# Kernel optimization log

Measured on AMD Instinct MI355X. Metric: run time of the kernel, lower is better.

The kernel has to match this reference:

```python
import jax, jax.numpy as jnp
import numpy as np

B = 32768
E = 10  # number of motion experts


def _p(k, shape, scale=0.05):
    return jax.random.normal(k, shape, dtype=jnp.float32) * scale


def setup_inputs() -> dict:
    key = jax.random.key(0)
    ks = jax.random.split(key, 24)
    inp = {"input_": jax.random.normal(ks[0], (B, 556), dtype=jnp.float32)}
    # encoder 0: pose 400 -> 512 -> 512
    inp["e0_W0"] = _p(ks[1], (400, 512)); inp["e0_b0"] = jnp.zeros((512,), jnp.float32)
    inp["e0_W1"] = _p(ks[2], (512, 512)); inp["e0_b1"] = jnp.zeros((512,), jnp.float32)
    # encoder 1: goal 78 -> 128 -> 128
    inp["e1_W0"] = _p(ks[3], (78, 128)); inp["e1_b0"] = jnp.zeros((128,), jnp.float32)
    inp["e1_W1"] = _p(ks[4], (128, 128)); inp["e1_b1"] = jnp.zeros((128,), jnp.float32)
    # gating NN (1 expert => plain MLP): 78 -> 512 -> 512 -> 10, softmax
    inp["g_W0"] = _p(ks[5], (78, 512)); inp["g_b0"] = jnp.zeros((512,), jnp.float32)
    inp["g_W1"] = _p(ks[6], (512, 512)); inp["g_b1"] = jnp.zeros((512,), jnp.float32)
    inp["g_W2"] = _p(ks[7], (512, 10)); inp["g_b2"] = jnp.zeros((10,), jnp.float32)
    # motion prediction ComponentNN: 10 experts, 640 -> 512 -> 512 -> 578
    inp["m_W0"] = _p(ks[8], (E, 640, 512)); inp["m_b0"] = jnp.zeros((E, 512), jnp.float32)
    inp["m_W1"] = _p(ks[9], (E, 512, 512)); inp["m_b1"] = jnp.zeros((E, 512), jnp.float32)
    inp["m_W2"] = _p(ks[10], (E, 512, 578)); inp["m_b2"] = jnp.zeros((E, 578), jnp.float32)
    return inp


def _expert_layer(x, w, W, b):
    # sum_e w[b,e] * (x[b] @ W[e] + b[e]); blend outputs (equiv. to blending weights)
    return jnp.einsum('be,bi,eio->bo', w, x, W) + w @ b


def reference(input_, e0_W0, e0_b0, e0_W1, e0_b1, e1_W0, e1_b0, e1_W1, e1_b1,
              g_W0, g_b0, g_W1, g_b1, g_W2, g_b2,
              m_W0, m_b0, m_W1, m_b1, m_W2, m_b2):
    elu = jax.nn.elu
    pose = input_[:, 0:400]
    goal = input_[:, 400:478]
    gate_in = input_[:, 478:556]
    # encoders (dropout inactive at inference)
    h0 = elu(elu(pose @ e0_W0 + e0_b0) @ e0_W1 + e0_b1)   # [B,512]
    h1 = elu(elu(goal @ e1_W0 + e1_b0) @ e1_W1 + e1_b1)   # [B,128]
    # gating: softmax over 10 experts
    g = elu(gate_in @ g_W0 + g_b0)
    g = elu(g @ g_W1 + g_b1)
    w = jax.nn.softmax(g @ g_W2 + g_b2, axis=-1)          # [B,10]
    feat = jnp.concatenate([h0, h1], axis=-1)             # [B,640]
    x = elu(_expert_layer(feat, w, m_W0, m_b0))
    x = elu(_expert_layer(x, w, m_W1, m_b1))
    pred = _expert_layer(x, w, m_W2, m_b2)                # [B,578], linear final
    return pred
```

## Files before the change

### kernel.cpp

```cpp
#include <hip/hip_runtime.h>
#include <math.h>

typedef _Float16 h8 __attribute__((ext_vector_type(8)));
typedef float f4 __attribute__((ext_vector_type(4)));

#define BATCH 32768

__device__ __forceinline__ void gload16(const void* g, void* l) {
  __builtin_amdgcn_global_load_lds(
      (const __attribute__((address_space(1))) unsigned int*)g,
      (__attribute__((address_space(3))) unsigned int*)l, 16, 0, 0);
}

__global__ __launch_bounds__(256) void prep_input2_k(const float* __restrict__ in,
    _Float16* __restrict__ pose, _Float16* __restrict__ goal, _Float16* __restrict__ gate)
{
  const long long total = (long long)BATCH * 88;
  for (long long i = (long long)blockIdx.x * 256 + threadIdx.x; i < total;
       i += (long long)gridDim.x * 256) {
    const int b = (int)(i / 88);
    const int g = (int)(i % 88);
    const float* r = in + (size_t)b * 556;
    h8 v;
    if (g < 56) {
      const int c0 = g * 8;
      #pragma unroll
      for (int j = 0; j < 8; ++j) {
        const int c = c0 + j;
        v[j] = (_Float16)((c < 400) ? r[c] : (c == 400 ? 1.0f : 0.0f));
      }
      *reinterpret_cast<h8*>(pose + (size_t)b * 448 + c0) = v;
    } else if (g < 72) {
      const int c0 = (g - 56) * 8;
      #pragma unroll
      for (int j = 0; j < 8; ++j) {
        const int c = c0 + j;
        v[j] = (_Float16)((c < 78) ? r[400 + c] : (c == 78 ? 1.0f : 0.0f));
      }
      *reinterpret_cast<h8*>(goal + (size_t)b * 128 + c0) = v;
    } else {
      const int c0 = (g - 72) * 8;
      #pragma unroll
      for (int j = 0; j < 8; ++j) {
        const int c = c0 + j;
        v[j] = (_Float16)((c < 78) ? r[478 + c] : (c == 78 ? 1.0f : 0.0f));
      }
      *reinterpret_cast<h8*>(gate + (size_t)b * 128 + c0) = v;
    }
  }
}

__global__ __launch_bounds__(256) void prep_wt_k(const float* __restrict__ W,
    const float* __restrict__ bias, _Float16* __restrict__ out,
    int K, int N, int Nld, int Kout, int biasCols, int biasLd)
{
  __shared__ float tile[64 * 65];
  const int t = threadIdx.x;
  const int c0 = blockIdx.x * 64;
  const int n0 = blockIdx.y * 64;
  {
    const int nn = t & 63;
    #pragma unroll
    for (int i = 0; i < 16; ++i) {
      int cc = (t >> 6) + i * 4;
      int c = c0 + cc, n = n0 + nn;
      float v = 0.0f;
      if (n < N) {
        if (c < K) v = W[(size_t)c * Nld + n];
        else if (c - K < biasCols) v = bias[(size_t)(c - K) * biasLd + n];
      }
      tile[cc * 65 + nn] = v;
    }
  }
  __syncthreads();
  {
    const int cc = t & 63;
    #pragma unroll
    for (int i = 0; i < 16; ++i) {
      int nn = (t >> 6) + i * 4;
      out[(size_t)(n0 + nn) * Kout + c0 + cc] = (_Float16)tile[cc * 65 + nn];
    }
  }
}

template<bool EPI_BIAS, bool DO_ELU, bool OUT_F32>
__global__ __launch_bounds__(256, 2) void gemm_k(
    const _Float16* __restrict__ A, const _Float16* __restrict__ Bw,
    void* __restrict__ OutP, const float* __restrict__ bias,
    int ldA, int ldB, int ldO, int nChunks, int nLimit)
{
  __shared__ __align__(16) _Float16 As[2][128 * 64];
  __shared__ __align__(16) _Float16 Bs[2][128 * 64];

  const int t = threadIdx.x;
  const int m0 = blockIdx.x * 128;
  const int n0 = blockIdx.y * 128;
  const int wid = t >> 6;
  const int lane = t & 63;
  const int wm = (wid >> 1) * 64;
  const int wn = (wid & 1) * 64;
  const int lr = lane & 15;
  const int lg = lane >> 4;

  const int gr = lane >> 3;
  const int gcol = ((lane & 7) ^ gr) * 8;
  const _Float16* Abase = A + (size_t)(m0 + wid * 32 + gr) * ldA + gcol;
  const _Float16* Bbase = Bw + (size_t)(n0 + wid * 32 + gr) * ldB + gcol;

  f4 acc[4][4];
  #pragma unroll
  for (int i = 0; i < 4; ++i)
    #pragma unroll
    for (int j = 0; j < 4; ++j) { f4 z = {0.f, 0.f, 0.f, 0.f}; acc[i][j] = z; }

  auto issue = [&](int c, int buf) {
    #pragma unroll
    for (int i = 0; i < 4; ++i) {
      gload16(Abase + (size_t)(i * 8) * ldA + c * 64, &As[buf][(wid * 32 + i * 8) * 64]);
      gload16(Bbase + (size_t)(i * 8) * ldB + c * 64, &Bs[buf][(wid * 32 + i * 8) * 64]);
    }
  };

  auto mfma_step = [&](const _Float16* as, const _Float16* bs) {
    #pragma unroll
    for (int kk = 0; kk < 2; ++kk) {
      h8 af[4], bf[4];
      const int kslot = kk * 4 + lg;
      #pragma unroll
      for (int i = 0; i < 4; ++i) {
        const int row = wm + i * 16 + lr;
        af[i] = *reinterpret_cast<const h8*>(&as[row * 64 + ((kslot ^ (row & 7)) << 3)]);
      }
      #pragma unroll
      for (int j = 0; j < 4; ++j) {
        const int row = wn + j * 16 + lr;
        bf[j] = *reinterpret_cast<const h8*>(&bs[row * 64 + ((kslot ^ (row & 7)) << 3)]);
      }
      #pragma unroll
      for (int i = 0; i < 4; ++i)
        #pragma unroll
        for (int j = 0; j < 4; ++j)
          acc[i][j] = __builtin_amdgcn_mfma_f32_16x16x32_f16(af[i], bf[j], acc[i][j], 0, 0, 0);
    }
  };

  issue(0, 0);
  int cur = 0;
  for (int c = 0; c < nChunks; ++c) {
    __syncthreads();
    if (c + 1 < nChunks) issue(c + 1, cur ^ 1);
    mfma_step(As[cur], Bs[cur]);
    cur ^= 1;
  }

  #pragma unroll
  for (int j = 0; j < 4; ++j) {
    const int col = n0 + wn + j * 16 + lr;
    if (col >= nLimit) continue;
    float bvv = 0.0f;
    if (EPI_BIAS) bvv = bias[col];
    #pragma unroll
    for (int i = 0; i < 4; ++i) {
      const int rowb = m0 + wm + i * 16 + lg * 4;
      #pragma unroll
      for (int r = 0; r < 4; ++r) {
        float x = acc[i][j][r] + bvv;
        if (DO_ELU) x = (x > 0.0f) ? x : expm1f(x);
        if (OUT_F32)
          reinterpret_cast<float*>(OutP)[(size_t)(rowb + r) * ldO + col] = x;
        else
          reinterpret_cast<_Float16*>(OutP)[(size_t)(rowb + r) * ldO + col] = (_Float16)x;
      }
    }
  }
}

template<int KCe, bool DO_ELU, bool OUT_F32>
__global__ __launch_bounds__(256, 4) void expertH_k(
    const _Float16* __restrict__ A, const _Float16* __restrict__ Bw,
    void* __restrict__ OutP, const _Float16* __restrict__ wpad,
    int ldA, int ldB, int ldO, int nLimit)
{
  constexpr int E = 10;
  __shared__ __align__(16) _Float16 lds[16384 + 1280];
  _Float16* Bs = lds;
  _Float16* wT = lds + 16384;

  const int tid = threadIdx.x;
  const int w = tid >> 6;
  const int l = tid & 63;
  const int m0 = blockIdx.x * 128;
  const int n0 = blockIdx.y * 128;
  const int lr = l & 15;
  const int lg = l >> 4;

  const int strow = tid >> 3;
  const int scol = ((tid & 7) ^ (strow & 7)) * 8;

  auto stB = [&](int buf, size_t colEl) {
    _Float16* d = Bs + buf * 8192 + w * 512;
    const _Float16* s = Bw + (size_t)(n0 + strow) * ldB + colEl + scol;
    #pragma unroll
    for (int p = 0; p < 4; ++p)
      gload16(s + (size_t)(p * 32) * ldB, d + p * 2048);
  };

  auto frag = [&](const _Float16* base, int row, int kslot) -> h8 {
    return *reinterpret_cast<const h8*>(base + row * 64 + ((kslot ^ (row & 7)) << 3));
  };

  h8 araw[2][2];
  auto loadA = [&](const _Float16* base, size_t ld, size_t col0) {
    #pragma unroll
    for (int kk = 0; kk < 2; ++kk)
      #pragma unroll
      for (int mi = 0; mi < 2; ++mi)
        araw[kk][mi] = *reinterpret_cast<const h8*>(
            base + (size_t)(m0 + w * 32 + mi * 16 + lr) * ld + col0 + (size_t)(kk * 4 + lg) * 8);
  };

  f4 acc[2][8];
  #pragma unroll
  for (int mi = 0; mi < 2; ++mi)
    #pragma unroll
    for (int ni = 0; ni < 8; ++ni) { f4 z = {0.f, 0.f, 0.f, 0.f}; acc[mi][ni] = z; }

  #pragma unroll
  for (int idx = tid; idx < 1280; idx += 256) {
    const int m = idx & 127, e = idx >> 7;
    wT[e * 128 + m] = wpad[(size_t)(m0 + m) * 64 + e];
  }
  loadA(A, (size_t)ldA, 0);
  stB(0, 0);
  asm volatile("s_waitcnt vmcnt(0) lgkmcnt(0)" ::: "memory");
  __builtin_amdgcn_s_barrier();
  __builtin_amdgcn_sched_barrier(0);

  int s = 0;
  #pragma unroll 1
  for (int kc = 0; kc < KCe; ++kc) {
    #pragma unroll 1
    for (int e = 0; e < E; ++e, ++s) {
      const _Float16* Bh = Bs + (s & 1) * 8192;

      if (e + 1 < E)         stB((s + 1) & 1, (size_t)((e + 1) * KCe + kc) * 64);
      else if (kc + 1 < KCe) stB((s + 1) & 1, (size_t)(kc + 1) * 64);
      else                   stB((s + 1) & 1, (size_t)(E * KCe) * 64);
      __builtin_amdgcn_sched_barrier(0);

      _Float16 se[2];
      #pragma unroll
      for (int j = 0; j < 2; ++j) se[j] = wT[e * 128 + w * 32 + j * 16 + lr];

      #pragma unroll
      for (int kk = 0; kk < 2; ++kk) {
        h8 aa[2];
        #pragma unroll
        for (int mi = 0; mi < 2; ++mi) {
          h8 v = araw[kk][mi];
          const _Float16 sv = se[mi];
          #pragma unroll
          for (int q = 0; q < 8; ++q) v[q] = v[q] * sv;
          aa[mi] = v;
        }
        #pragma unroll
        for (int c0 = 0; c0 < 8; c0 += 4) {
          h8 bf[4];
          #pragma unroll
          for (int ni = 0; ni < 4; ++ni)
            bf[ni] = frag(Bh, (c0 + ni) * 16 + lr, kk * 4 + lg);
          __builtin_amdgcn_s_setprio(1);
          #pragma unroll
          for (int mi = 0; mi < 2; ++mi)
            #pragma unroll
            for (int ni = 0; ni < 4; ++ni)
              acc[mi][c0 + ni] =
                  __builtin_amdgcn_mfma_f32_16x16x32_f16(aa[mi], bf[ni], acc[mi][c0 + ni], 0, 0, 0);
          __builtin_amdgcn_s_setprio(0);
        }
      }

      __builtin_amdgcn_sched_barrier(0);
      asm volatile("s_waitcnt vmcnt(0)" ::: "memory");
      __builtin_amdgcn_s_barrier();
      __builtin_amdgcn_sched_barrier(0);
    }
    if (kc + 1 < KCe) loadA(A, (size_t)ldA, (size_t)(kc + 1) * 64);
    else              loadA(wpad, 64, 0);
  }

  {
    const _Float16* Bh = Bs + (s & 1) * 8192;
    #pragma unroll
    for (int kk = 0; kk < 2; ++kk) {
      #pragma unroll
      for (int c0 = 0; c0 < 8; c0 += 4) {
        h8 bf[4];
        #pragma unroll
        for (int ni = 0; ni < 4; ++ni)
          bf[ni] = frag(Bh, (c0 + ni) * 16 + lr, kk * 4 + lg);
        #pragma unroll
        for (int mi = 0; mi < 2; ++mi)
          #pragma unroll
          for (int ni = 0; ni < 4; ++ni)
            acc[mi][c0 + ni] =
                __builtin_amdgcn_mfma_f32_16x16x32_f16(araw[kk][mi], bf[ni], acc[mi][c0 + ni], 0, 0, 0);
      }
    }
  }

  #pragma unroll
  for (int ni = 0; ni < 8; ++ni) {
    const int col = n0 + ni * 16 + lr;
    if (col >= nLimit) continue;
    #pragma unroll
    for (int mi = 0; mi < 2; ++mi) {
      const int rowb = m0 + w * 32 + mi * 16 + lg * 4;
      #pragma unroll
      for (int r = 0; r < 4; ++r) {
        float x = acc[mi][ni][r];
        if (DO_ELU) x = (x > 0.0f) ? x : expm1f(x);
        if (OUT_F32)
          reinterpret_cast<float*>(OutP)[(size_t)(rowb + r) * ldO + col] = x;
        else
          reinterpret_cast<_Float16*>(OutP)[(size_t)(rowb + r) * ldO + col] = (_Float16)x;
      }
    }
  }
}

template<int KCe, int NI, bool DO_ELU, bool OUT_F32>
__global__ __launch_bounds__(256, 2) void expertV_k(
    const _Float16* __restrict__ A, const _Float16* __restrict__ Bw,
    void* __restrict__ OutP, const _Float16* __restrict__ wpad,
    int ldA, int ldB, int ldO, int nLimit)
{
  constexpr int E = 10;
  constexpr int S = KCe * E + 1;
  constexpr int SG = NI / 2;
  constexpr int SLOT = NI * 1024;
  __shared__ __align__(16) _Float16 lds[3 * SLOT + 2560];
  _Float16* wT = lds + 3 * SLOT;

  const int tid = threadIdx.x;
  const int w = tid >> 6;
  const int l = tid & 63;
  const int m0 = blockIdx.x * 256;
  const int n0 = blockIdx.y * (NI * 16);
  const int lr = l & 15;
  const int lg = l >> 4;

  const int strow = tid >> 3;
  const int scol = ((tid & 7) ^ (strow & 7)) * 8;

  auto stB = [&](int slot, size_t colEl) {
    _Float16* d = lds + slot * SLOT + w * 512;
    const _Float16* sp = Bw + (size_t)(n0 + strow) * ldB + colEl + scol;
    #pragma unroll
    for (int p = 0; p < SG; ++p)
      gload16(sp + (size_t)(p * 32) * ldB, d + p * 2048);
  };

  auto frag = [&](const _Float16* base, int row, int kslot) -> h8 {
    return *reinterpret_cast<const h8*>(base + row * 64 + ((kslot ^ (row & 7)) << 3));
  };

  h8 araw[2][4];
  auto loadA = [&](const _Float16* base, size_t ld, size_t col0) {
    #pragma unroll
    for (int kk = 0; kk < 2; ++kk)
      #pragma unroll
      for (int mi = 0; mi < 4; ++mi)
        araw[kk][mi] = *reinterpret_cast<const h8*>(
            base + (size_t)(m0 + w * 64 + mi * 16 + lr) * ld + col0 + (size_t)(kk * 4 + lg) * 8);
  };

  f4 acc[4][NI];
  #pragma unroll
  for (int mi = 0; mi < 4; ++mi)
    #pragma unroll
    for (int ni = 0; ni < NI; ++ni) { f4 z = {0.f, 0.f, 0.f, 0.f}; acc[mi][ni] = z; }

  #pragma unroll
  for (int idx = tid; idx < 2560; idx += 256) {
    const int m = idx & 255, e = idx >> 8;
    wT[e * 256 + m] = wpad[(size_t)(m0 + m) * 64 + e];
  }
  loadA(A, (size_t)ldA, 0);
  stB(0, 0);
  stB(1, (size_t)KCe * 64);
  if constexpr (SG == 4) asm volatile("s_waitcnt vmcnt(4)" ::: "memory");
  else                   asm volatile("s_waitcnt vmcnt(5)" ::: "memory");
  asm volatile("s_waitcnt lgkmcnt(0)" ::: "memory");
  __builtin_amdgcn_s_barrier();
  __builtin_amdgcn_sched_barrier(0);

  int e_s = 0, kc_s = 0;
  int e_t = 2, kc_t = 0;
  #pragma unroll 1
  for (int s = 0; s < S; ++s) {
    const _Float16* Bh = lds + (s % 3) * SLOT;

    if (s + 2 < S) {
      const size_t col = (kc_t < KCe) ? (size_t)(e_t * KCe + kc_t) * 64
                                      : (size_t)(E * KCe) * 64;
      stB((s + 2) % 3, col);
    }
    __builtin_amdgcn_sched_barrier(0);

    const bool isBias = (kc_s == KCe);
    _Float16 se[4];
    if (!isBias) {
      #pragma unroll
      for (int j = 0; j < 4; ++j) se[j] = wT[e_s * 256 + w * 64 + j * 16 + lr];
    }

    #pragma unroll
    for (int kk = 0; kk < 2; ++kk) {
      h8 aa[4];
      #pragma unroll
      for (int mi = 0; mi < 4; ++mi) {
        h8 v = araw[kk][mi];
        if (!isBias) {
          const _Float16 sv = se[mi];
          #pragma unroll
          for (int q = 0; q < 8; ++q) v[q] = v[q] * sv;
        }
        aa[mi] = v;
      }
      #pragma unroll
      for (int c0 = 0; c0 < NI; c0 += 4) {
        h8 bf[4];
        #pragma unroll
        for (int ni = 0; ni < 4; ++ni)
          if (c0 + ni < NI) bf[ni] = frag(Bh, (c0 + ni) * 16 + lr, kk * 4 + lg);
        __builtin_amdgcn_s_setprio(1);
        #pragma unroll
        for (int mi = 0; mi < 4; ++mi)
          #pragma unroll
          for (int ni = 0; ni < 4; ++ni)
            if (c0 + ni < NI)
              acc[mi][c0 + ni] =
                  __builtin_amdgcn_mfma_f32_16x16x32_f16(aa[mi], bf[ni], acc[mi][c0 + ni], 0, 0, 0);
        __builtin_amdgcn_s_setprio(0);
      }
    }
    __builtin_amdgcn_sched_barrier(0);

    if (s + 1 < S) {
      if (s + 2 < S) {
        if constexpr (SG == 4) asm volatile("s_waitcnt vmcnt(4)" ::: "memory");
        else                   asm volatile("s_waitcnt vmcnt(5)" ::: "memory");
      } else {
        asm volatile("s_waitcnt vmcnt(0)" ::: "memory");
      }
      __builtin_amdgcn_s_barrier();
      __builtin_amdgcn_sched_barrier(0);
      if (e_s == E - 1) {
        if (kc_s + 1 < KCe) loadA(A, (size_t)ldA, (size_t)(kc_s + 1) * 64);
        else                loadA(wpad, 64, 0);
        e_s = 0; ++kc_s;
      } else ++e_s;
      if (kc_t < KCe) { if (e_t == E - 1) { e_t = 0; ++kc_t; } else ++e_t; }
    }
  }

  #pragma unroll
  for (int ni = 0; ni < NI; ++ni) {
    const int col = n0 + ni * 16 + lr;
    if (col >= nLimit) continue;
    #pragma unroll
    for (int mi = 0; mi < 4; ++mi) {
      const int rowb = m0 + w * 64 + mi * 16 + lg * 4;
      #pragma unroll
      for (int r = 0; r < 4; ++r) {
        float x = acc[mi][ni][r];
        if (DO_ELU) x = (x > 0.0f) ? x : expm1f(x);
        if (OUT_F32)
          reinterpret_cast<float*>(OutP)[(size_t)(rowb + r) * ldO + col] = x;
        else
          reinterpret_cast<_Float16*>(OutP)[(size_t)(rowb + r) * ldO + col] = (_Float16)x;
      }
    }
  }
}

__global__ __launch_bounds__(256) void gate_softmax_k(const _Float16* __restrict__ gb,
    const float* __restrict__ W2, const float* __restrict__ b2, _Float16* __restrict__ wpad)
{
  __shared__ float W2s[5120];
  for (int i = threadIdx.x; i < 5120; i += 256) W2s[i] = W2[i];
  __syncthreads();
  const int t = threadIdx.x;
  const int sub = t & 3;
  const int b = blockIdx.x * 64 + (t >> 2);
  const _Float16* row = gb + (size_t)b * 512 + sub * 128;
  float acc[10];
  #pragma unroll
  for (int o = 0; o < 10; ++o) acc[o] = 0.0f;
  #pragma unroll 4
  for (int k0 = 0; k0 < 128; k0 += 8) {
    h8 x = *reinterpret_cast<const h8*>(row + k0);
    #pragma unroll
    for (int jj = 0; jj < 8; ++jj) {
      float xv = (float)x[jj];
      const int k = sub * 128 + k0 + jj;
      #pragma unroll
      for (int o = 0; o < 10; ++o) acc[o] += xv * W2s[k * 10 + o];
    }
  }
  #pragma unroll
  for (int o = 0; o < 10; ++o) {
    acc[o] += __shfl_xor(acc[o], 1);
    acc[o] += __shfl_xor(acc[o], 2);
    acc[o] += b2[o];
  }
  float mx = acc[0];
  #pragma unroll
  for (int o = 1; o < 10; ++o) mx = fmaxf(mx, acc[o]);
  float s = 0.0f;
  #pragma unroll
  for (int o = 0; o < 10; ++o) { acc[o] = expf(acc[o] - mx); s += acc[o]; }
  const float inv = 1.0f / s;
  h8 o0 = {0,0,0,0,0,0,0,0}, o1 = {0,0,0,0,0,0,0,0};
  if (sub == 0) {
    #pragma unroll
    for (int o = 0; o < 8; ++o) o0[o] = (_Float16)(acc[o] * inv);
    o1[0] = (_Float16)(acc[8] * inv);
    o1[1] = (_Float16)(acc[9] * inv);
  }
  _Float16* wr = wpad + (size_t)b * 64 + sub * 16;
  *reinterpret_cast<h8*>(wr) = o0;
  *reinterpret_cast<h8*>(wr + 8) = o1;
}

extern "C" void kernel_launch(void* const* d_in, const int* in_sizes, int n_in,
                              void* d_out, int out_size, void* d_ws, size_t ws_size,
                              hipStream_t stream)
{
  const float* input_ = (const float*)d_in[0];
  const float* e0_W0 = (const float*)d_in[1];
  const float* e0_b0 = (const float*)d_in[2];
  const float* e0_W1 = (const float*)d_in[3];
  const float* e0_b1 = (const float*)d_in[4];
  const float* e1_W0 = (const float*)d_in[5];
  const float* e1_b0 = (const float*)d_in[6];
  const float* e1_W1 = (const float*)d_in[7];
  const float* e1_b1 = (const float*)d_in[8];
  const float* g_W0  = (const float*)d_in[9];
  const float* g_b0  = (const float*)d_in[10];
  const float* g_W1  = (const float*)d_in[11];
  const float* g_b1  = (const float*)d_in[12];
  const float* g_W2  = (const float*)d_in[13];
  const float* g_b2  = (const float*)d_in[14];
  const float* m_W0  = (const float*)d_in[15];
  const float* m_b0  = (const float*)d_in[16];
  const float* m_W1  = (const float*)d_in[17];
  const float* m_b1  = (const float*)d_in[18];
  const float* m_W2  = (const float*)d_in[19];
  const float* m_b2  = (const float*)d_in[20];
  (void)in_sizes; (void)n_in; (void)out_size; (void)ws_size;

  char* ws = (char*)d_ws;
  size_t off = 0;
  auto alloc = [&](size_t bytes) { char* p = ws + off; off += (bytes + 255) & ~(size_t)255; return p; };

  const size_t Bn = BATCH;
  _Float16* wsA    = (_Float16*)alloc(Bn * 512 * 2);
  _Float16* wsB    = (_Float16*)alloc(Bn * 512 * 2);
  _Float16* wsC    = (_Float16*)alloc(Bn * 640 * 2);
  _Float16* goal16 = (_Float16*)alloc(Bn * 128 * 2);
  _Float16* gate16 = (_Float16*)alloc(Bn * 128 * 2);
  _Float16* h1a16  = (_Float16*)alloc(Bn * 128 * 2);
  _Float16* wpad16 = (_Float16*)alloc(Bn * 64 * 2);
  _Float16* e0W0t  = (_Float16*)alloc((size_t)512 * 448 * 2);
  _Float16* e0W1t  = (_Float16*)alloc((size_t)512 * 512 * 2);
  _Float16* e1W0t  = (_Float16*)alloc((size_t)128 * 128 * 2);
  _Float16* e1W1t  = (_Float16*)alloc((size_t)128 * 128 * 2);
  _Float16* gW0t   = (_Float16*)alloc((size_t)512 * 128 * 2);
  _Float16* gW1t   = (_Float16*)alloc((size_t)512 * 512 * 2);
  _Float16* W0b    = (_Float16*)alloc((size_t)512 * 6464 * 2);
  _Float16* W1b    = (_Float16*)alloc((size_t)512 * 5184 * 2);
  _Float16* W2b    = (_Float16*)alloc((size_t)768 * 5184 * 2);

  dim3 blk(256);
  const int BIG = 1 << 30;

  prep_input2_k<<<dim3(2048), blk, 0, stream>>>(input_, wsA, goal16, gate16);

  prep_wt_k<<<dim3(7, 8),    blk, 0, stream>>>(e0_W0, e0_b0, e0W0t, 400, 512, 512, 448, 1, 0);
  prep_wt_k<<<dim3(8, 8),    blk, 0, stream>>>(e0_W1, nullptr, e0W1t, 512, 512, 512, 512, 0, 0);
  prep_wt_k<<<dim3(2, 2),    blk, 0, stream>>>(e1_W0, e1_b0, e1W0t, 78, 128, 128, 128, 1, 0);
  prep_wt_k<<<dim3(2, 2),    blk, 0, stream>>>(e1_W1, nullptr, e1W1t, 128, 128, 128, 128, 0, 0);
  prep_wt_k<<<dim3(2, 8),    blk, 0, stream>>>(g_W0, g_b0, gW0t, 78, 512, 512, 128, 1, 0);
  prep_wt_k<<<dim3(8, 8),    blk, 0, stream>>>(g_W1, nullptr, gW1t, 512, 512, 512, 512, 0, 0);
  prep_wt_k<<<dim3(101, 8),  blk, 0, stream>>>(m_W0, m_b0, W0b, 6400, 512, 512, 6464, 10, 512);
  prep_wt_k<<<dim3(81, 8),   blk, 0, stream>>>(m_W1, m_b1, W1b, 5120, 512, 512, 5184, 10, 512);
  prep_wt_k<<<dim3(81, 12),  blk, 0, stream>>>(m_W2, m_b2, W2b, 5120, 578, 578, 5184, 10, 578);

  gemm_k<false, true, false><<<dim3(256, 4), blk, 0, stream>>>(
      wsA, e0W0t, wsB, nullptr, 448, 448, 512, 7, BIG);
  gemm_k<true, true, false><<<dim3(256, 4), blk, 0, stream>>>(
      wsB, e0W1t, wsC, e0_b1, 512, 512, 640, 8, BIG);
  gemm_k<false, true, false><<<dim3(256, 1), blk, 0, stream>>>(
      goal16, e1W0t, h1a16, nullptr, 128, 128, 128, 2, BIG);
  gemm_k<true, true, false><<<dim3(256, 1), blk, 0, stream>>>(
      h1a16, e1W1t, wsC + 512, e1_b1, 128, 128, 640, 2, BIG);
  gemm_k<false, true, false><<<dim3(256, 4), blk, 0, stream>>>(
      gate16, gW0t, wsA, nullptr, 128, 128, 512, 2, BIG);
  gemm_k<true, true, false><<<dim3(256, 4), blk, 0, stream>>>(
      wsA, gW1t, wsB, g_b1, 512, 512, 512, 8, BIG);
  gate_softmax_k<<<dim3(BATCH / 64), blk, 0, stream>>>(wsB, g_W2, g_b2, wpad16);

  expertH_k<10, true, false><<<dim3(256, 4), blk, 0, stream>>>(
      wsC, W0b, wsA, wpad16, 640, 6464, 512, BIG);
  expertH_k<8, true, false><<<dim3(256, 4), blk, 0, stream>>>(
      wsA, W1b, wsC, wpad16, 512, 5184, 512, BIG);
  expertV_k<8, 10, false, true><<<dim3(128, 4), blk, 0, stream>>>(
      wsC, W2b, d_out, wpad16, 512, 5184, 578, 578);
}
```

Before: 875.1 us.

## Double expert-layer M tile, stage two experts per barrier, batch weight prep

The expert kernels for the first two layers now handle 256 rows per block instead of 128. Each pipeline step stages the weight tiles of two experts at once, which halves the barrier/wait count and doubles reuse of each B tile across rows. The nine per-weight transpose/convert launches are merged into one launch driven by a descriptor table. In exchange the kernel uses roughly 4x more LDS and twice the accumulator registers, drops to 2 blocks per CU, and launches half as many blocks.

```diff
diff --git a/kernel.cpp b/kernel.cpp
--- a/kernel.cpp
+++ b/kernel.cpp
@@ -50,24 +50,35 @@
   }
 }
 
-__global__ __launch_bounds__(256) void prep_wt_k(const float* __restrict__ W,
-    const float* __restrict__ bias, _Float16* __restrict__ out,
-    int K, int N, int Nld, int Kout, int biasCols, int biasLd)
+struct PrepDesc {
+  const float* W;
+  const float* bias;
+  _Float16* out;
+  int K, N, Nld, Kout, biasCols, biasLd;
+  int tilesX, tiles;
+};
+struct PrepAll { PrepDesc d[9]; };
+
+__global__ __launch_bounds__(256) void prep_wt_all_k(PrepAll p)
 {
   __shared__ float tile[64 * 65];
+  int bid = blockIdx.x;
+  int i = 0;
+  while (bid >= p.d[i].tiles) { bid -= p.d[i].tiles; ++i; }
+  const PrepDesc& d = p.d[i];
+  const int c0 = (bid % d.tilesX) * 64;
+  const int n0 = (bid / d.tilesX) * 64;
   const int t = threadIdx.x;
-  const int c0 = blockIdx.x * 64;
-  const int n0 = blockIdx.y * 64;
   {
     const int nn = t & 63;
     #pragma unroll
-    for (int i = 0; i < 16; ++i) {
-      int cc = (t >> 6) + i * 4;
+    for (int q = 0; q < 16; ++q) {
+      int cc = (t >> 6) + q * 4;
       int c = c0 + cc, n = n0 + nn;
       float v = 0.0f;
-      if (n < N) {
-        if (c < K) v = W[(size_t)c * Nld + n];
-        else if (c - K < biasCols) v = bias[(size_t)(c - K) * biasLd + n];
+      if (n < d.N) {
+        if (c < d.K) v = d.W[(size_t)c * d.Nld + n];
+        else if (c - d.K < d.biasCols) v = d.bias[(size_t)(c - d.K) * d.biasLd + n];
       }
       tile[cc * 65 + nn] = v;
     }
@@ -76,9 +87,9 @@
   {
     const int cc = t & 63;
     #pragma unroll
-    for (int i = 0; i < 16; ++i) {
-      int nn = (t >> 6) + i * 4;
-      out[(size_t)(n0 + nn) * Kout + c0 + cc] = (_Float16)tile[cc * 65 + nn];
+    for (int q = 0; q < 16; ++q) {
+      int nn = (t >> 6) + q * 4;
+      d.out[(size_t)(n0 + nn) * d.Kout + c0 + cc] = (_Float16)tile[cc * 65 + nn];
     }
   }
 }
@@ -176,20 +187,21 @@
 }
 
 template<int KCe, bool DO_ELU, bool OUT_F32>
-__global__ __launch_bounds__(256, 4) void expertH_k(
+__global__ __launch_bounds__(256, 2) void expertP2_k(
     const _Float16* __restrict__ A, const _Float16* __restrict__ Bw,
     void* __restrict__ OutP, const _Float16* __restrict__ wpad,
     int ldA, int ldB, int ldO, int nLimit)
 {
   constexpr int E = 10;
-  __shared__ __align__(16) _Float16 lds[16384 + 1280];
+  constexpr int NP = E / 2;
+  __shared__ __align__(16) _Float16 lds[65536 + 2560];
   _Float16* Bs = lds;
-  _Float16* wT = lds + 16384;
+  _Float16* wT = lds + 65536;
 
   const int tid = threadIdx.x;
   const int w = tid >> 6;
   const int l = tid & 63;
-  const int m0 = blockIdx.x * 128;
+  const int m0 = blockIdx.x * 256;
   const int n0 = blockIdx.y * 128;
   const int lr = l & 15;
   const int lg = l >> 4;
@@ -197,41 +209,42 @@
   const int strow = tid >> 3;
   const int scol = ((tid & 7) ^ (strow & 7)) * 8;
 
-  auto stB = [&](int buf, size_t colEl) {
-    _Float16* d = Bs + buf * 8192 + w * 512;
-    const _Float16* s = Bw + (size_t)(n0 + strow) * ldB + colEl + scol;
+  auto stB = [&](int buf, int win, size_t colEl) {
+    _Float16* d = Bs + buf * 32768 + win * 8192 + w * 512;
+    const _Float16* sp = Bw + (size_t)(n0 + strow) * ldB + colEl + scol;
     #pragma unroll
     for (int p = 0; p < 4; ++p)
-      gload16(s + (size_t)(p * 32) * ldB, d + p * 2048);
+      gload16(sp + (size_t)(p * 32) * ldB, d + p * 2048);
   };
 
   auto frag = [&](const _Float16* base, int row, int kslot) -> h8 {
     return *reinterpret_cast<const h8*>(base + row * 64 + ((kslot ^ (row & 7)) << 3));
   };
 
-  h8 araw[2][2];
+  h8 araw[2][4];
   auto loadA = [&](const _Float16* base, size_t ld, size_t col0) {
     #pragma unroll
     for (int kk = 0; kk < 2; ++kk)
       #pragma unroll
-      for (int mi = 0; mi < 2; ++mi)
+      for (int mi = 0; mi < 4; ++mi)
         araw[kk][mi] = *reinterpret_cast<const h8*>(
-            base + (size_t)(m0 + w * 32 + mi * 16 + lr) * ld + col0 + (size_t)(kk * 4 + lg) * 8);
-  };
-
-  f4 acc[2][8];
-  #pragma unroll
-  for (int mi = 0; mi < 2; ++mi)
+            base + (size_t)(m0 + w * 64 + mi * 16 + lr) * ld + col0 + (size_t)(kk * 4 + lg) * 8);
+  };
+
+  f4 acc[4][8];
+  #pragma unroll
+  for (int mi = 0; mi < 4; ++mi)
     #pragma unroll
     for (int ni = 0; ni < 8; ++ni) { f4 z = {0.f, 0.f, 0.f, 0.f}; acc[mi][ni] = z; }
 
   #pragma unroll
-  for (int idx = tid; idx < 1280; idx += 256) {
-    const int m = idx & 127, e = idx >> 7;
-    wT[e * 128 + m] = wpad[(size_t)(m0 + m) * 64 + e];
+  for (int idx = tid; idx < 2560; idx += 256) {
+    const int m = idx & 255, e = idx >> 8;
+    wT[e * 256 + m] = wpad[(size_t)(m0 + m) * 64 + e];
   }
   loadA(A, (size_t)ldA, 0);
-  stB(0, 0);
+  stB(0, 0, 0);
+  stB(0, 1, (size_t)KCe * 64);
   asm volatile("s_waitcnt vmcnt(0) lgkmcnt(0)" ::: "memory");
   __builtin_amdgcn_s_barrier();
   __builtin_amdgcn_sched_barrier(0);
@@ -240,43 +253,54 @@
   #pragma unroll 1
   for (int kc = 0; kc < KCe; ++kc) {
     #pragma unroll 1
-    for (int e = 0; e < E; ++e, ++s) {
-      const _Float16* Bh = Bs + (s & 1) * 8192;
-
-      if (e + 1 < E)         stB((s + 1) & 1, (size_t)((e + 1) * KCe + kc) * 64);
-      else if (kc + 1 < KCe) stB((s + 1) & 1, (size_t)(kc + 1) * 64);
-      else                   stB((s + 1) & 1, (size_t)(E * KCe) * 64);
+    for (int p = 0; p < NP; ++p, ++s) {
+      const _Float16* Bbuf = Bs + (s & 1) * 32768;
+      const int nbuf = (s + 1) & 1;
+
+      if (p + 1 < NP) {
+        stB(nbuf, 0, (size_t)((2 * p + 2) * KCe + kc) * 64);
+        stB(nbuf, 1, (size_t)((2 * p + 3) * KCe + kc) * 64);
+      } else if (kc + 1 < KCe) {
+        stB(nbuf, 0, (size_t)(kc + 1) * 64);
+        stB(nbuf, 1, (size_t)(KCe + kc + 1) * 64);
+      } else {
+        stB(nbuf, 0, (size_t)(E * KCe) * 64);
+      }
       __builtin_amdgcn_sched_barrier(0);
 
-      _Float16 se[2];
-      #pragma unroll
-      for (int j = 0; j < 2; ++j) se[j] = wT[e * 128 + w * 32 + j * 16 + lr];
-
-      #pragma unroll
-      for (int kk = 0; kk < 2; ++kk) {
-        h8 aa[2];
+      #pragma unroll
+      for (int sub = 0; sub < 2; ++sub) {
+        const int e = 2 * p + sub;
+        const _Float16* Bh = Bbuf + sub * 8192;
+        _Float16 se[4];
         #pragma unroll
-        for (int mi = 0; mi < 2; ++mi) {
-          h8 v = araw[kk][mi];
-          const _Float16 sv = se[mi];
+        for (int j = 0; j < 4; ++j) se[j] = wT[e * 256 + w * 64 + j * 16 + lr];
+        #pragma unroll
+        for (int kk = 0; kk < 2; ++kk) {
+          h8 aa[4];
           #pragma unroll
-          for (int q = 0; q < 8; ++q) v[q] = v[q] * sv;
-          aa[mi] = v;
-        }
-        #pragma unroll
-        for (int c0 = 0; c0 < 8; c0 += 4) {
-          h8 bf[4];
+          for (int mi = 0; mi < 4; ++mi) {
+            h8 v = araw[kk][mi];
+            const _Float16 sv = se[mi];
+            #pragma unroll
+            for (int q = 0; q < 8; ++q) v[q] = v[q] * sv;
+            aa[mi] = v;
+          }
           #pragma unroll
-          for (int ni = 0; ni < 4; ++ni)
-            bf[ni] = frag(Bh, (c0 + ni) * 16 + lr, kk * 4 + lg);
-          __builtin_amdgcn_s_setprio(1);
-          #pragma unroll
-          for (int mi = 0; mi < 2; ++mi)
+          for (int c0 = 0; c0 < 8; c0 += 4) {
+            h8 bf[4];
             #pragma unroll
             for (int ni = 0; ni < 4; ++ni)
-              acc[mi][c0 + ni] =
-                  __builtin_amdgcn_mfma_f32_16x16x32_f16(aa[mi], bf[ni], acc[mi][c0 + ni], 0, 0, 0);
-          __builtin_amdgcn_s_setprio(0);
+              bf[ni] = frag(Bh, (c0 + ni) * 16 + lr, kk * 4 + lg);
+            __builtin_amdgcn_s_setprio(1);
+            #pragma unroll
+            for (int mi = 0; mi < 4; ++mi)
+              #pragma unroll
+              for (int ni = 0; ni < 4; ++ni)
+                acc[mi][c0 + ni] =
+                    __builtin_amdgcn_mfma_f32_16x16x32_f16(aa[mi], bf[ni], acc[mi][c0 + ni], 0, 0, 0);
+            __builtin_amdgcn_s_setprio(0);
+          }
         }
       }
 
@@ -290,7 +314,7 @@
   }
 
   {
-    const _Float16* Bh = Bs + (s & 1) * 8192;
+    const _Float16* Bh = Bs + (s & 1) * 32768;
     #pragma unroll
     for (int kk = 0; kk < 2; ++kk) {
       #pragma unroll
@@ -300,7 +324,7 @@
         for (int ni = 0; ni < 4; ++ni)
           bf[ni] = frag(Bh, (c0 + ni) * 16 + lr, kk * 4 + lg);
         #pragma unroll
-        for (int mi = 0; mi < 2; ++mi)
+        for (int mi = 0; mi < 4; ++mi)
           #pragma unroll
           for (int ni = 0; ni < 4; ++ni)
             acc[mi][c0 + ni] =
@@ -314,8 +338,8 @@
     const int col = n0 + ni * 16 + lr;
     if (col >= nLimit) continue;
     #pragma unroll
-    for (int mi = 0; mi < 2; ++mi) {
-      const int rowb = m0 + w * 32 + mi * 16 + lg * 4;
+    for (int mi = 0; mi < 4; ++mi) {
+      const int rowb = m0 + w * 64 + mi * 16 + lg * 4;
       #pragma unroll
       for (int r = 0; r < 4; ++r) {
         float x = acc[mi][ni][r];
@@ -588,15 +612,28 @@
 
   prep_input2_k<<<dim3(2048), blk, 0, stream>>>(input_, wsA, goal16, gate16);
 
-  prep_wt_k<<<dim3(7, 8),    blk, 0, stream>>>(e0_W0, e0_b0, e0W0t, 400, 512, 512, 448, 1, 0);
-  prep_wt_k<<<dim3(8, 8),    blk, 0, stream>>>(e0_W1, nullptr, e0W1t, 512, 512, 512, 512, 0, 0);
-  prep_wt_k<<<dim3(2, 2),    blk, 0, stream>>>(e1_W0, e1_b0, e1W0t, 78, 128, 128, 128, 1, 0);
-  prep_wt_k<<<dim3(2, 2),    blk, 0, stream>>>(e1_W1, nullptr, e1W1t, 128, 128, 128, 128, 0, 0);
-  prep_wt_k<<<dim3(2, 8),    blk, 0, stream>>>(g_W0, g_b0, gW0t, 78, 512, 512, 128, 1, 0);
-  prep_wt_k<<<dim3(8, 8),    blk, 0, stream>>>(g_W1, nullptr, gW1t, 512, 512, 512, 512, 0, 0);
-  prep_wt_k<<<dim3(101, 8),  blk, 0, stream>>>(m_W0, m_b0, W0b, 6400, 512, 512, 6464, 10, 512);
-  prep_wt_k<<<dim3(81, 8),   blk, 0, stream>>>(m_W1, m_b1, W1b, 5120, 512, 512, 5184, 10, 512);
-  prep_wt_k<<<dim3(81, 12),  blk, 0, stream>>>(m_W2, m_b2, W2b, 5120, 578, 578, 5184, 10, 578);
+  {
+    PrepAll p;
+    auto mk = [](const float* W, const float* bias, _Float16* out,
+                 int K, int N, int Nld, int Kout, int biasCols, int biasLd,
+                 int tx, int ty) {
+      PrepDesc d; d.W = W; d.bias = bias; d.out = out; d.K = K; d.N = N; d.Nld = Nld;
+      d.Kout = Kout; d.biasCols = biasCols; d.biasLd = biasLd; d.tilesX = tx; d.tiles = tx * ty;
+      return d;
+    };
+    p.d[0] = mk(e0_W0, e0_b0, e0W0t, 400, 512, 512, 448, 1, 0, 7, 8);
+    p.d[1] = mk(e0_W1, nullptr, e0W1t, 512, 512, 512, 512, 0, 0, 8, 8);
+    p.d[2] = mk(e1_W0, e1_b0, e1W0t, 78, 128, 128, 128, 1, 0, 2, 2);
+    p.d[3] = mk(e1_W1, nullptr, e1W1t, 128, 128, 128, 128, 0, 0, 2, 2);
+    p.d[4] = mk(g_W0, g_b0, gW0t, 78, 512, 512, 128, 1, 0, 2, 8);
+    p.d[5] = mk(g_W1, nullptr, gW1t, 512, 512, 512, 512, 0, 0, 8, 8);
+    p.d[6] = mk(m_W0, m_b0, W0b, 6400, 512, 512, 6464, 10, 512, 101, 8);
+    p.d[7] = mk(m_W1, m_b1, W1b, 5120, 512, 512, 5184, 10, 512, 81, 8);
+    p.d[8] = mk(m_W2, m_b2, W2b, 5120, 578, 578, 5184, 10, 578, 81, 12);
+    int total = 0;
+    for (int i = 0; i < 9; ++i) total += p.d[i].tiles;
+    prep_wt_all_k<<<dim3(total), blk, 0, stream>>>(p);
+  }
 
   gemm_k<false, true, false><<<dim3(256, 4), blk, 0, stream>>>(
       wsA, e0W0t, wsB, nullptr, 448, 448, 512, 7, BIG);
@@ -612,9 +649,9 @@
       wsA, gW1t, wsB, g_b1, 512, 512, 512, 8, BIG);
   gate_softmax_k<<<dim3(BATCH / 64), blk, 0, stream>>>(wsB, g_W2, g_b2, wpad16);
 
-  expertH_k<10, true, false><<<dim3(256, 4), blk, 0, stream>>>(
+  expertP2_k<10, true, false><<<dim3(128, 4), blk, 0, stream>>>(
       wsC, W0b, wsA, wpad16, 640, 6464, 512, BIG);
-  expertH_k<8, true, false><<<dim3(256, 4), blk, 0, stream>>>(
+  expertP2_k<8, true, false><<<dim3(128, 4), blk, 0, stream>>>(
       wsA, W1b, wsC, wpad16, 512, 5184, 512, BIG);
   expertV_k<8, 10, false, true><<<dim3(128, 4), blk, 0, stream>>>(
       wsC, W2b, d_out, wpad16, 512, 5184, 578, 578);
```

Measured after the change: 851.9 us. 2.7% less time.
